# Optimization experiments

Measured on AMD Instinct MI355X. Metric: run time of the kernel, lower is better.

Reference implementation:

```python
import jax, jax.numpy as jnp
import numpy as np
import math

L, B, E, H = 1024, 16, 512, 8
NUM_REL = 2 * L - 1  # 2047


def setup_inputs() -> dict:
    key = jax.random.key(0)
    ks = jax.random.split(key, 9)
    s = 0.02
    query = jax.random.normal(ks[0], (L, B, E), dtype=jnp.float32)
    return {
        "query": query,
        "key": jax.random.normal(ks[1], (L, B, E), dtype=jnp.float32),
        "value": jax.random.normal(ks[2], (L, B, E), dtype=jnp.float32),
        "in_proj_weight": jax.random.normal(ks[3], (3 * E, E), dtype=jnp.float32) * s,
        "in_proj_bias": jax.random.normal(ks[4], (3 * E,), dtype=jnp.float32) * s,
        "out_proj_weight": jax.random.normal(ks[5], (E, E), dtype=jnp.float32) * s,
        "out_proj_bias": jax.random.normal(ks[6], (E,), dtype=jnp.float32) * s,
        "rpe_weight_table": jax.random.normal(ks[7], (H, NUM_REL), dtype=jnp.float32) * s,
        "rpe_indices": jax.random.randint(ks[8], (L, L), 0, NUM_REL, dtype=jnp.int32),
    }


def _heads(x, w, b):
    # x: (N, Bn, E), w: (E, E), b: (E,) -> (Bn, H, N, d)
    n, bn, e = x.shape
    d = e // H
    y = jnp.einsum('nbe,fe->nbf', x, w) + b
    return y.reshape(n, bn, H, d).transpose(1, 2, 0, 3)


def reference(query, key, value, in_proj_weight, in_proj_bias, out_proj_weight,
              out_proj_bias, rpe_weight_table, rpe_indices):
    l, bn, e = query.shape
    d = e // H
    wq, wk, wv = jnp.split(in_proj_weight, 3, axis=0)
    bq, bk, bv = jnp.split(in_proj_bias, 3, axis=0)
    q = _heads(query, wq, bq)   # (B, H, L, d)
    k = _heads(key, wk, bk)     # (B, H, S, d)
    v = _heads(value, wv, bv)   # (B, H, S, d)
    q = q / math.sqrt(d)
    # rel-pos bias: gather table -> (H, L, S), broadcast over batch
    bias = rpe_weight_table[:, rpe_indices]
    attn = jnp.einsum('bhld,bhsd->bhls', q, k) + bias[None]
    attn = jax.nn.softmax(attn, axis=-1)
    out = jnp.einsum('bhls,bhsd->bhld', attn, v)   # (B, H, L, d)
    out = out.transpose(2, 0, 1, 3).reshape(l, bn, e)  # (L, B, E)
    out = jnp.einsum('lbe,fe->lbf', out, out_proj_weight) + out_proj_bias
    return out
```

## Files before the change

kernel.cpp:

```cpp
#include <hip/hip_runtime.h>
#include <hip/hip_bf16.h>


#define L_SEQ 1024
#define B_N   16
#define E_DIM 512
#define H_N   8
#define NREL  2047

typedef _Float16 f16;
using half8   = __attribute__((ext_vector_type(8))) _Float16;
using floatx4 = __attribute__((ext_vector_type(4))) float;

__device__ __forceinline__ half8 cvt8(const float4 a, const float4 b) {
    half8 h;
    h[0] = (f16)a.x; h[1] = (f16)a.y; h[2] = (f16)a.z; h[3] = (f16)a.w;
    h[4] = (f16)b.x; h[5] = (f16)b.y; h[6] = (f16)b.z; h[7] = (f16)b.w;
    return h;
}

__device__ __forceinline__ void gl_lds16(const void* g, void* l) {
    __builtin_amdgcn_global_load_lds(
        (const __attribute__((address_space(1))) unsigned int*)g,
        (__attribute__((address_space(3))) unsigned int*)l,
        16, 0, 0);
}

__global__ __launch_bounds__(256) void qkv_kernel(
    const float* __restrict__ Xq, const float* __restrict__ Xk, const float* __restrict__ Xv,
    const float* __restrict__ W, const float* __restrict__ Bias,
    f16* __restrict__ Qo, f16* __restrict__ Ko, f16* __restrict__ Vo)
{
    const int flat = blockIdx.x;
    const int xcd  = flat & 7;
    const int slot = flat >> 3;
    const int g    = xcd * 48 + (slot >> 2);
    const int f0   = (slot & 3) << 7;
    const int proj = g >> 7;
    const int n0   = (g & 127) << 7;

    const float* X  = (proj == 0) ? Xq : (proj == 1) ? Xk : Xv;
    const float* Wp = W + (size_t)(proj << 9) * E_DIM;

    __shared__ __align__(16) float As[128 * 32];
    __shared__ __align__(16) float Bs[128 * 32];

    const int tid  = threadIdx.x;
    const int w    = tid >> 6;
    const int lane = tid & 63;
    const int quad = lane >> 4, c = lane & 15;
    const int wm = (w >> 1) << 6, wn = (w & 1) << 6;

    const int lr = lane >> 3;
    const int lc = (lane & 7) ^ lr;
    const float* Xg = X  + (size_t)(n0 + (w << 3) + lr) * E_DIM + (lc << 2);
    const float* Wg = Wp + (size_t)(f0 + (w << 3) + lr) * E_DIM + (lc << 2);

    const int sa0 = (((quad << 1) ^ (c & 7)) << 2);
    const int sa1 = sa0 ^ 4;

    floatx4 acc[4][4] = {};

    for (int k0 = 0; k0 < E_DIM; k0 += 32) {
        __syncthreads();
#pragma unroll
        for (int i = 0; i < 4; ++i) {
            gl_lds16(Xg + (size_t)i * (32 * E_DIM) + k0, &As[((i << 5) + (w << 3)) << 5]);
            gl_lds16(Wg + (size_t)i * (32 * E_DIM) + k0, &Bs[((i << 5) + (w << 3)) << 5]);
        }
        __syncthreads();

        half8 a[4], bfr[4];
#pragma unroll
        for (int mt = 0; mt < 4; ++mt) {
            const int r = (wm + mt * 16 + c) << 5;
            const float4 lo = *reinterpret_cast<const float4*>(&As[r + sa0]);
            const float4 hi = *reinterpret_cast<const float4*>(&As[r + sa1]);
            a[mt] = cvt8(lo, hi);
        }
#pragma unroll
        for (int nt = 0; nt < 4; ++nt) {
            const int r = (wn + nt * 16 + c) << 5;
            const float4 lo = *reinterpret_cast<const float4*>(&Bs[r + sa0]);
            const float4 hi = *reinterpret_cast<const float4*>(&Bs[r + sa1]);
            bfr[nt] = cvt8(lo, hi);
        }
#pragma unroll
        for (int mt = 0; mt < 4; ++mt)
#pragma unroll
            for (int nt = 0; nt < 4; ++nt)
                acc[mt][nt] = __builtin_amdgcn_mfma_f32_16x16x32_f16(a[mt], bfr[nt], acc[mt][nt], 0, 0, 0);
    }

    f16* Dst = (proj == 0) ? Qo : (proj == 1) ? Ko : Vo;
    const float scale = (proj == 0) ? 0.125f : 1.0f;

#pragma unroll
    for (int nt = 0; nt < 4; ++nt) {
        const int fl = f0 + wn + nt * 16 + c;
        const float bj = Bias[(proj << 9) + fl];
        const int h = fl >> 6, d = fl & 63;
#pragma unroll
        for (int mt = 0; mt < 4; ++mt) {
#pragma unroll
            for (int r = 0; r < 4; ++r) {
                const int n = n0 + wm + mt * 16 + quad * 4 + r;
                const int l = n >> 4, b = n & 15;
                Dst[((((size_t)b * H_N + h) * L_SEQ + l) << 6) + d] =
                    (f16)((acc[mt][nt][r] + bj) * scale);
            }
        }
    }
}

__global__ __launch_bounds__(256) void transpose_v(
    const f16* __restrict__ V, f16* __restrict__ Vt)
{
    const int l0 = blockIdx.x << 6;
    const size_t base = (size_t)blockIdx.y << 16;
    __shared__ __align__(16) f16 T[64][72];
    const int tid = threadIdx.x;
    const int r = tid >> 2, co = (tid & 3) << 4;

    const uint4 a0 = *reinterpret_cast<const uint4*>(V + base + (size_t)(l0 + r) * 64 + co);
    const uint4 a1 = *reinterpret_cast<const uint4*>(V + base + (size_t)(l0 + r) * 64 + co + 8);
    *reinterpret_cast<uint4*>(&T[r][co])     = a0;
    *reinterpret_cast<uint4*>(&T[r][co + 8]) = a1;
    __syncthreads();

    union { f16 h[16]; uint4 u[2]; } pk;
#pragma unroll
    for (int j = 0; j < 16; ++j) pk.h[j] = T[co + j][r];
    *reinterpret_cast<uint4*>(Vt + base + (size_t)r * 1024 + l0 + co)     = pk.u[0];
    *reinterpret_cast<uint4*>(Vt + base + (size_t)r * 1024 + l0 + co + 8) = pk.u[1];
}

__global__ __launch_bounds__(256, 3) void attn_kernel(
    const f16* __restrict__ Q, const f16* __restrict__ K, const f16* __restrict__ Vt,
    const int* __restrict__ RPE, const float* __restrict__ Tab, f16* __restrict__ CTX)
{
    const int q0 = blockIdx.x << 7;
    const int bh = blockIdx.y;
    const int b = bh >> 3, h = bh & 7;

    const int tid  = threadIdx.x;
    const int w    = tid >> 6;
    const int lane = tid & 63;
    const int quad = lane >> 4, c = lane & 15;

    __shared__ __align__(16) f16 Ks[64][72];
    __shared__ __align__(16) f16 Vts[64][72];
    __shared__ __align__(16) f16 Pw[4][32][72];
    __shared__ float tab[NREL];

    const size_t base = (size_t)bh << 16;

    for (int i = tid; i < NREL; i += 256) tab[i] = Tab[h * NREL + i];

    const int qg0 = q0 + (w << 5);
    half8 Aq[2][2];
#pragma unroll
    for (int s = 0; s < 2; ++s) {
        const f16* qp = Q + base + (size_t)(qg0 + s * 16 + c) * 64 + quad * 8;
        Aq[s][0] = *reinterpret_cast<const half8*>(qp);
        Aq[s][1] = *reinterpret_cast<const half8*>(qp + 32);
    }

    floatx4 o[2][4] = {};
    float l_part[2][4] = {};

    const int* rp = RPE + (size_t)(qg0 + (quad << 2)) * 1024 + c;

    const int sr = tid >> 2, so = (tid & 3) << 4;
    const f16* kbase = K  + base + (size_t)sr * 64 + so;
    const f16* vbase = Vt + base + (size_t)sr * 1024 + so;

    uint4 pk0 = *reinterpret_cast<const uint4*>(kbase);
    uint4 pk1 = *reinterpret_cast<const uint4*>(kbase + 8);
    uint4 pv0 = *reinterpret_cast<const uint4*>(vbase);
    uint4 pv1 = *reinterpret_cast<const uint4*>(vbase + 8);

    for (int j0 = 0; j0 < L_SEQ; j0 += 64) {
        __syncthreads();
        *reinterpret_cast<uint4*>(&Ks[sr][so])      = pk0;
        *reinterpret_cast<uint4*>(&Ks[sr][so + 8])  = pk1;
        *reinterpret_cast<uint4*>(&Vts[sr][so])     = pv0;
        *reinterpret_cast<uint4*>(&Vts[sr][so + 8]) = pv1;
        __syncthreads();

        if (j0 + 64 < L_SEQ) {
            const f16* kn = kbase + (size_t)(j0 + 64) * 64;
            const f16* vn = vbase + (j0 + 64);
            pk0 = *reinterpret_cast<const uint4*>(kn);
            pk1 = *reinterpret_cast<const uint4*>(kn + 8);
            pv0 = *reinterpret_cast<const uint4*>(vn);
            pv1 = *reinterpret_cast<const uint4*>(vn + 8);
        }

        int idx[2][4][4];
#pragma unroll
        for (int s = 0; s < 2; ++s)
#pragma unroll
            for (int r = 0; r < 4; ++r)
#pragma unroll
                for (int nt = 0; nt < 4; ++nt)
                    idx[s][r][nt] = rp[(size_t)(s * 16 + r) * 1024 + j0 + nt * 16];

        floatx4 sc[2][4];
#pragma unroll
        for (int nt = 0; nt < 4; ++nt) {
            const half8 b0 = *reinterpret_cast<const half8*>(&Ks[nt * 16 + c][quad * 8]);
            const half8 b1 = *reinterpret_cast<const half8*>(&Ks[nt * 16 + c][32 + quad * 8]);
            floatx4 t0 = {}, t1 = {};
            t0 = __builtin_amdgcn_mfma_f32_16x16x32_f16(Aq[0][0], b0, t0, 0, 0, 0);
            t0 = __builtin_amdgcn_mfma_f32_16x16x32_f16(Aq[0][1], b1, t0, 0, 0, 0);
            t1 = __builtin_amdgcn_mfma_f32_16x16x32_f16(Aq[1][0], b0, t1, 0, 0, 0);
            t1 = __builtin_amdgcn_mfma_f32_16x16x32_f16(Aq[1][1], b1, t1, 0, 0, 0);
            sc[0][nt] = t0; sc[1][nt] = t1;
        }

#pragma unroll
        for (int s = 0; s < 2; ++s)
#pragma unroll
            for (int r = 0; r < 4; ++r) {
                float rs = 0.0f;
#pragma unroll
                for (int nt = 0; nt < 4; ++nt) {
                    const float p = __expf(sc[s][nt][r] + tab[idx[s][r][nt]]);
                    rs += p;
                    Pw[w][s * 16 + quad * 4 + r][nt * 16 + c] = (f16)p;
                }
                l_part[s][r] += rs;
            }

        half8 vb[4][2];
#pragma unroll
        for (int nt = 0; nt < 4; ++nt) {
            vb[nt][0] = *reinterpret_cast<const half8*>(&Vts[nt * 16 + c][quad * 8]);
            vb[nt][1] = *reinterpret_cast<const half8*>(&Vts[nt * 16 + c][32 + quad * 8]);
        }
#pragma unroll
        for (int s = 0; s < 2; ++s) {
            const half8 Ap0 = *reinterpret_cast<const half8*>(&Pw[w][s * 16 + c][quad * 8]);
            const half8 Ap1 = *reinterpret_cast<const half8*>(&Pw[w][s * 16 + c][32 + quad * 8]);
#pragma unroll
            for (int nt = 0; nt < 4; ++nt) {
                o[s][nt] = __builtin_amdgcn_mfma_f32_16x16x32_f16(Ap0, vb[nt][0], o[s][nt], 0, 0, 0);
                o[s][nt] = __builtin_amdgcn_mfma_f32_16x16x32_f16(Ap1, vb[nt][1], o[s][nt], 0, 0, 0);
            }
        }
    }

#pragma unroll
    for (int s = 0; s < 2; ++s)
#pragma unroll
        for (int r = 0; r < 4; ++r) {
            float l = l_part[s][r];
            l += __shfl_xor(l, 1); l += __shfl_xor(l, 2);
            l += __shfl_xor(l, 4); l += __shfl_xor(l, 8);
            const float inv = 1.0f / l;
            const int lrow = qg0 + s * 16 + quad * 4 + r;
            f16* dp = CTX + ((size_t)(lrow * 16 + b)) * 512 + h * 64;
#pragma unroll
            for (int nt = 0; nt < 4; ++nt)
                dp[nt * 16 + c] = (f16)(o[s][nt][r] * inv);
        }
}

__global__ __launch_bounds__(256) void out_kernel(
    const f16* __restrict__ X, const float* __restrict__ W, const float* __restrict__ Bias,
    float* __restrict__ Out)
{
    const int flat = blockIdx.x;
    const int xcd  = flat & 7;
    const int slot = flat >> 3;
    const int m    = xcd * 16 + (slot >> 2);
    const int f0   = (slot & 3) << 7;
    const int n0   = m << 7;

    __shared__ __align__(16) f16   As[128 * 32];
    __shared__ __align__(16) float Bs[128 * 32];

    const int tid  = threadIdx.x;
    const int w    = tid >> 6;
    const int lane = tid & 63;
    const int quad = lane >> 4, c = lane & 15;
    const int wm = (w >> 1) << 6, wn = (w & 1) << 6;

    const int ar  = lane >> 2;
    const int ac  = (lane & 3) ^ ((lane >> 3) & 3);
    const f16* Xg = X + (size_t)(n0 + (w << 4) + ar) * E_DIM + (ac << 3);

    const int lr = lane >> 3;
    const int lc = (lane & 7) ^ lr;
    const float* Wg = W + (size_t)(f0 + (w << 3) + lr) * E_DIM + (lc << 2);

    const int sa = ((quad ^ ((c >> 1) & 3)) << 3);
    const int sb0 = (((quad << 1) ^ (c & 7)) << 2);
    const int sb1 = sb0 ^ 4;

    floatx4 acc[4][4] = {};

    for (int k0 = 0; k0 < E_DIM; k0 += 32) {
        __syncthreads();
#pragma unroll
        for (int i = 0; i < 2; ++i)
            gl_lds16(Xg + (size_t)i * (64 * E_DIM) + k0, &As[((i << 6) + (w << 4)) << 5]);
#pragma unroll
        for (int i = 0; i < 4; ++i)
            gl_lds16(Wg + (size_t)i * (32 * E_DIM) + k0, &Bs[((i << 5) + (w << 3)) << 5]);
        __syncthreads();

        half8 a[4], bfr[4];
#pragma unroll
        for (int mt = 0; mt < 4; ++mt) {
            const int r = (wm + mt * 16 + c) << 5;
            a[mt] = *reinterpret_cast<const half8*>(&As[r + sa]);
        }
#pragma unroll
        for (int nt = 0; nt < 4; ++nt) {
            const int r = (wn + nt * 16 + c) << 5;
            const float4 lo = *reinterpret_cast<const float4*>(&Bs[r + sb0]);
            const float4 hi = *reinterpret_cast<const float4*>(&Bs[r + sb1]);
            bfr[nt] = cvt8(lo, hi);
        }
#pragma unroll
        for (int mt = 0; mt < 4; ++mt)
#pragma unroll
            for (int nt = 0; nt < 4; ++nt)
                acc[mt][nt] = __builtin_amdgcn_mfma_f32_16x16x32_f16(a[mt], bfr[nt], acc[mt][nt], 0, 0, 0);
    }

#pragma unroll
    for (int nt = 0; nt < 4; ++nt) {
        const int f = f0 + wn + nt * 16 + c;
        const float bj = Bias[f];
#pragma unroll
        for (int mt = 0; mt < 4; ++mt) {
#pragma unroll
            for (int r = 0; r < 4; ++r) {
                const int n = n0 + wm + mt * 16 + quad * 4 + r;
                Out[(size_t)n * E_DIM + f] = acc[mt][nt][r] + bj;
            }
        }
    }
}

extern "C" void kernel_launch(void* const* d_in, const int* in_sizes, int n_in,
                              void* d_out, int out_size, void* d_ws, size_t ws_size,
                              hipStream_t stream) {
    const float* q_in = (const float*)d_in[0];
    const float* k_in = (const float*)d_in[1];
    const float* v_in = (const float*)d_in[2];
    const float* ipw  = (const float*)d_in[3];
    const float* ipb  = (const float*)d_in[4];
    const float* opw  = (const float*)d_in[5];
    const float* opb  = (const float*)d_in[6];
    const float* tab  = (const float*)d_in[7];
    const int*   rpe  = (const int*)d_in[8];
    float* out = (float*)d_out;

    f16* ws   = (f16*)d_ws;
    f16* Q    = ws;
    f16* K    = ws + 8388608;
    f16* Vt   = ws + 16777216;
    f16* Vtmp = ws + 25165824;
    f16* CTX  = ws + 25165824;

    qkv_kernel<<<dim3(1536), 256, 0, stream>>>(q_in, k_in, v_in, ipw, ipb, Q, K, Vtmp);
    transpose_v<<<dim3(16, 128), 256, 0, stream>>>(Vtmp, Vt);
    attn_kernel<<<dim3(8, 128), 256, 0, stream>>>(Q, K, Vt, rpe, tab, CTX);
    out_kernel<<<dim3(512), 256, 0, stream>>>(CTX, opw, opb, out);
}
```

Measured before the change: 320.4 us.

## Double-buffer GEMM LDS tiles and load attention K/V straight into registers

The QKV and output projection GEMMs now keep two LDS buffers and prefetch the next k-slice with global_load_lds while the current one is computed, leaving one barrier per iteration instead of two. The attention kernel drops its shared K/V staging: each wave loads its K and V fragments directly from global memory into registers and skips the per-tile barriers. Blocks are remapped to a flat grid that spreads batch-heads across XCDs, and the occupancy hint of 3 blocks is removed. In exchange, LDS per GEMM block doubles and the four attention waves now read the same K/V tiles redundantly from cache, which may raise cache traffic and register pressure.

```diff
diff --git a/kernel.cpp b/kernel.cpp
--- a/kernel.cpp
+++ b/kernel.cpp
@@ -42,8 +42,8 @@
     const float* X  = (proj == 0) ? Xq : (proj == 1) ? Xk : Xv;
     const float* Wp = W + (size_t)(proj << 9) * E_DIM;
 
-    __shared__ __align__(16) float As[128 * 32];
-    __shared__ __align__(16) float Bs[128 * 32];
+    __shared__ __align__(16) float As[2][128 * 32];
+    __shared__ __align__(16) float Bs[2][128 * 32];
 
     const int tid  = threadIdx.x;
     const int w    = tid >> 6;
@@ -59,30 +59,36 @@
     const int sa0 = (((quad << 1) ^ (c & 7)) << 2);
     const int sa1 = sa0 ^ 4;
 
+    auto stage = [&](int buf, int kk) {
+#pragma unroll
+        for (int i = 0; i < 4; ++i) {
+            gl_lds16(Xg + (size_t)i * (32 * E_DIM) + kk, &As[buf][((i << 5) + (w << 3)) << 5]);
+            gl_lds16(Wg + (size_t)i * (32 * E_DIM) + kk, &Bs[buf][((i << 5) + (w << 3)) << 5]);
+        }
+    };
+
     floatx4 acc[4][4] = {};
 
+    stage(0, 0);
+    __syncthreads();
+
+    int cur = 0;
     for (int k0 = 0; k0 < E_DIM; k0 += 32) {
-        __syncthreads();
-#pragma unroll
-        for (int i = 0; i < 4; ++i) {
-            gl_lds16(Xg + (size_t)i * (32 * E_DIM) + k0, &As[((i << 5) + (w << 3)) << 5]);
-            gl_lds16(Wg + (size_t)i * (32 * E_DIM) + k0, &Bs[((i << 5) + (w << 3)) << 5]);
-        }
-        __syncthreads();
+        if (k0 + 32 < E_DIM) stage(cur ^ 1, k0 + 32);
 
         half8 a[4], bfr[4];
 #pragma unroll
         for (int mt = 0; mt < 4; ++mt) {
             const int r = (wm + mt * 16 + c) << 5;
-            const float4 lo = *reinterpret_cast<const float4*>(&As[r + sa0]);
-            const float4 hi = *reinterpret_cast<const float4*>(&As[r + sa1]);
+            const float4 lo = *reinterpret_cast<const float4*>(&As[cur][r + sa0]);
+            const float4 hi = *reinterpret_cast<const float4*>(&As[cur][r + sa1]);
             a[mt] = cvt8(lo, hi);
         }
 #pragma unroll
         for (int nt = 0; nt < 4; ++nt) {
             const int r = (wn + nt * 16 + c) << 5;
-            const float4 lo = *reinterpret_cast<const float4*>(&Bs[r + sa0]);
-            const float4 hi = *reinterpret_cast<const float4*>(&Bs[r + sa1]);
+            const float4 lo = *reinterpret_cast<const float4*>(&Bs[cur][r + sa0]);
+            const float4 hi = *reinterpret_cast<const float4*>(&Bs[cur][r + sa1]);
             bfr[nt] = cvt8(lo, hi);
         }
 #pragma unroll
@@ -90,6 +96,9 @@
 #pragma unroll
             for (int nt = 0; nt < 4; ++nt)
                 acc[mt][nt] = __builtin_amdgcn_mfma_f32_16x16x32_f16(a[mt], bfr[nt], acc[mt][nt], 0, 0, 0);
+
+        __syncthreads();
+        cur ^= 1;
     }
 
     f16* Dst = (proj == 0) ? Qo : (proj == 1) ? Ko : Vo;
@@ -135,12 +144,15 @@
     *reinterpret_cast<uint4*>(Vt + base + (size_t)r * 1024 + l0 + co + 8) = pk.u[1];
 }
 
-__global__ __launch_bounds__(256, 3) void attn_kernel(
+__global__ __launch_bounds__(256) void attn_kernel(
     const f16* __restrict__ Q, const f16* __restrict__ K, const f16* __restrict__ Vt,
     const int* __restrict__ RPE, const float* __restrict__ Tab, f16* __restrict__ CTX)
 {
-    const int q0 = blockIdx.x << 7;
-    const int bh = blockIdx.y;
+    const int flat = blockIdx.x;
+    const int xcd  = flat & 7;
+    const int slot = flat >> 3;
+    const int q0   = (slot & 7) << 7;
+    const int bh   = ((slot >> 3) << 3) + xcd;
     const int b = bh >> 3, h = bh & 7;
 
     const int tid  = threadIdx.x;
@@ -148,8 +160,6 @@
     const int lane = tid & 63;
     const int quad = lane >> 4, c = lane & 15;
 
-    __shared__ __align__(16) f16 Ks[64][72];
-    __shared__ __align__(16) f16 Vts[64][72];
     __shared__ __align__(16) f16 Pw[4][32][72];
     __shared__ float tab[NREL];
 
@@ -165,36 +175,25 @@
         Aq[s][0] = *reinterpret_cast<const half8*>(qp);
         Aq[s][1] = *reinterpret_cast<const half8*>(qp + 32);
     }
+    __syncthreads();
 
     floatx4 o[2][4] = {};
     float l_part[2][4] = {};
 
     const int* rp = RPE + (size_t)(qg0 + (quad << 2)) * 1024 + c;
-
-    const int sr = tid >> 2, so = (tid & 3) << 4;
-    const f16* kbase = K  + base + (size_t)sr * 64 + so;
-    const f16* vbase = Vt + base + (size_t)sr * 1024 + so;
-
-    uint4 pk0 = *reinterpret_cast<const uint4*>(kbase);
-    uint4 pk1 = *reinterpret_cast<const uint4*>(kbase + 8);
-    uint4 pv0 = *reinterpret_cast<const uint4*>(vbase);
-    uint4 pv1 = *reinterpret_cast<const uint4*>(vbase + 8);
+    const f16* Kp = K  + base;
+    const f16* Vp = Vt + base;
 
     for (int j0 = 0; j0 < L_SEQ; j0 += 64) {
-        __syncthreads();
-        *reinterpret_cast<uint4*>(&Ks[sr][so])      = pk0;
-        *reinterpret_cast<uint4*>(&Ks[sr][so + 8])  = pk1;
-        *reinterpret_cast<uint4*>(&Vts[sr][so])     = pv0;
-        *reinterpret_cast<uint4*>(&Vts[sr][so + 8]) = pv1;
-        __syncthreads();
-
-        if (j0 + 64 < L_SEQ) {
-            const f16* kn = kbase + (size_t)(j0 + 64) * 64;
-            const f16* vn = vbase + (j0 + 64);
-            pk0 = *reinterpret_cast<const uint4*>(kn);
-            pk1 = *reinterpret_cast<const uint4*>(kn + 8);
-            pv0 = *reinterpret_cast<const uint4*>(vn);
-            pv1 = *reinterpret_cast<const uint4*>(vn + 8);
+        half8 kb[4][2], vb[4][2];
+#pragma unroll
+        for (int nt = 0; nt < 4; ++nt) {
+            const f16* kp = Kp + (size_t)(j0 + nt * 16 + c) * 64 + quad * 8;
+            kb[nt][0] = *reinterpret_cast<const half8*>(kp);
+            kb[nt][1] = *reinterpret_cast<const half8*>(kp + 32);
+            const f16* vp = Vp + (size_t)(nt * 16 + c) * 1024 + j0 + quad * 8;
+            vb[nt][0] = *reinterpret_cast<const half8*>(vp);
+            vb[nt][1] = *reinterpret_cast<const half8*>(vp + 32);
         }
 
         int idx[2][4][4];
@@ -209,13 +208,11 @@
         floatx4 sc[2][4];
 #pragma unroll
         for (int nt = 0; nt < 4; ++nt) {
-            const half8 b0 = *reinterpret_cast<const half8*>(&Ks[nt * 16 + c][quad * 8]);
-            const half8 b1 = *reinterpret_cast<const half8*>(&Ks[nt * 16 + c][32 + quad * 8]);
             floatx4 t0 = {}, t1 = {};
-            t0 = __builtin_amdgcn_mfma_f32_16x16x32_f16(Aq[0][0], b0, t0, 0, 0, 0);
-            t0 = __builtin_amdgcn_mfma_f32_16x16x32_f16(Aq[0][1], b1, t0, 0, 0, 0);
-            t1 = __builtin_amdgcn_mfma_f32_16x16x32_f16(Aq[1][0], b0, t1, 0, 0, 0);
-            t1 = __builtin_amdgcn_mfma_f32_16x16x32_f16(Aq[1][1], b1, t1, 0, 0, 0);
+            t0 = __builtin_amdgcn_mfma_f32_16x16x32_f16(Aq[0][0], kb[nt][0], t0, 0, 0, 0);
+            t0 = __builtin_amdgcn_mfma_f32_16x16x32_f16(Aq[0][1], kb[nt][1], t0, 0, 0, 0);
+            t1 = __builtin_amdgcn_mfma_f32_16x16x32_f16(Aq[1][0], kb[nt][0], t1, 0, 0, 0);
+            t1 = __builtin_amdgcn_mfma_f32_16x16x32_f16(Aq[1][1], kb[nt][1], t1, 0, 0, 0);
             sc[0][nt] = t0; sc[1][nt] = t1;
         }
 
@@ -233,12 +230,6 @@
                 l_part[s][r] += rs;
             }
 
-        half8 vb[4][2];
-#pragma unroll
-        for (int nt = 0; nt < 4; ++nt) {
-            vb[nt][0] = *reinterpret_cast<const half8*>(&Vts[nt * 16 + c][quad * 8]);
-            vb[nt][1] = *reinterpret_cast<const half8*>(&Vts[nt * 16 + c][32 + quad * 8]);
-        }
 #pragma unroll
         for (int s = 0; s < 2; ++s) {
             const half8 Ap0 = *reinterpret_cast<const half8*>(&Pw[w][s * 16 + c][quad * 8]);
@@ -278,8 +269,8 @@
     const int f0   = (slot & 3) << 7;
     const int n0   = m << 7;
 
-    __shared__ __align__(16) f16   As[128 * 32];
-    __shared__ __align__(16) float Bs[128 * 32];
+    __shared__ __align__(16) f16   As[2][128 * 32];
+    __shared__ __align__(16) float Bs[2][128 * 32];
 
     const int tid  = threadIdx.x;
     const int w    = tid >> 6;
@@ -299,29 +290,35 @@
     const int sb0 = (((quad << 1) ^ (c & 7)) << 2);
     const int sb1 = sb0 ^ 4;
 
+    auto stage = [&](int buf, int kk) {
+#pragma unroll
+        for (int i = 0; i < 2; ++i)
+            gl_lds16(Xg + (size_t)i * (64 * E_DIM) + kk, &As[buf][((i << 6) + (w << 4)) << 5]);
+#pragma unroll
+        for (int i = 0; i < 4; ++i)
+            gl_lds16(Wg + (size_t)i * (32 * E_DIM) + kk, &Bs[buf][((i << 5) + (w << 3)) << 5]);
+    };
+
     floatx4 acc[4][4] = {};
 
+    stage(0, 0);
+    __syncthreads();
+
+    int cur = 0;
     for (int k0 = 0; k0 < E_DIM; k0 += 32) {
-        __syncthreads();
-#pragma unroll
-        for (int i = 0; i < 2; ++i)
-            gl_lds16(Xg + (size_t)i * (64 * E_DIM) + k0, &As[((i << 6) + (w << 4)) << 5]);
-#pragma unroll
-        for (int i = 0; i < 4; ++i)
-            gl_lds16(Wg + (size_t)i * (32 * E_DIM) + k0, &Bs[((i << 5) + (w << 3)) << 5]);
-        __syncthreads();
+        if (k0 + 32 < E_DIM) stage(cur ^ 1, k0 + 32);
 
         half8 a[4], bfr[4];
 #pragma unroll
         for (int mt = 0; mt < 4; ++mt) {
             const int r = (wm + mt * 16 + c) << 5;
-            a[mt] = *reinterpret_cast<const half8*>(&As[r + sa]);
+            a[mt] = *reinterpret_cast<const half8*>(&As[cur][r + sa]);
         }
 #pragma unroll
         for (int nt = 0; nt < 4; ++nt) {
             const int r = (wn + nt * 16 + c) << 5;
-            const float4 lo = *reinterpret_cast<const float4*>(&Bs[r + sb0]);
-            const float4 hi = *reinterpret_cast<const float4*>(&Bs[r + sb1]);
+            const float4 lo = *reinterpret_cast<const float4*>(&Bs[cur][r + sb0]);
+            const float4 hi = *reinterpret_cast<const float4*>(&Bs[cur][r + sb1]);
             bfr[nt] = cvt8(lo, hi);
         }
 #pragma unroll
@@ -329,6 +326,9 @@
 #pragma unroll
             for (int nt = 0; nt < 4; ++nt)
                 acc[mt][nt] = __builtin_amdgcn_mfma_f32_16x16x32_f16(a[mt], bfr[nt], acc[mt][nt], 0, 0, 0);
+
+        __syncthreads();
+        cur ^= 1;
     }
 
 #pragma unroll
@@ -369,6 +369,6 @@
 
     qkv_kernel<<<dim3(1536), 256, 0, stream>>>(q_in, k_in, v_in, ipw, ipb, Q, K, Vtmp);
     transpose_v<<<dim3(16, 128), 256, 0, stream>>>(Vtmp, Vt);
-    attn_kernel<<<dim3(8, 128), 256, 0, stream>>>(Q, K, Vt, rpe, tab, CTX);
+    attn_kernel<<<dim3(1024), 256, 0, stream>>>(Q, K, Vt, rpe, tab, CTX);
     out_kernel<<<dim3(512), 256, 0, stream>>>(CTX, opw, opb, out);
 }
```

New measurement: 378.2 us. 18.0% more time.
